# Kernel tuning notes

Hardware: AMD Instinct MI355X
Metric: run time of the kernel (lower is better)

Reference implementation:

```python
import jax, jax.numpy as jnp
import numpy as np
import itertools


def setup_inputs() -> dict:
    key = jax.random.key(0)
    k1, k2 = jax.random.split(key)
    # Learned 3D LUT: [3, D, D, D], values in [0,1] like an identity/learned color LUT
    lut = jax.random.uniform(k1, (3, 33, 33, 33), dtype=jnp.float32)
    # Input RGB image batch in [0,1): [B, 3, H, W]
    x = jax.random.uniform(k2, (4, 3, 1080, 1920), dtype=jnp.float32)
    return {"lut": lut, "x": x}


def reference(lut, x):
    # Faithful JAX version of the trilinear.forward CUDA kernel:
    # per-pixel 8-corner trilinear interpolation into a [3, D, D, D] LUT.
    dim = lut.shape[-1]
    binsize = 1.000001 / (dim - 1)

    r, g, b = x[:, 0], x[:, 1], x[:, 2]  # each [B, H, W]

    inv = 1.0 / binsize
    rid = jnp.floor(r * inv).astype(jnp.int32)
    gid = jnp.floor(g * inv).astype(jnp.int32)
    bid = jnp.floor(b * inv).astype(jnp.int32)
    # fractional offsets within the cell
    fr = r * inv - rid
    fg = g * inv - gid
    fb = b * inv - bid
    # clamp so id+1 stays in range (kernel assumes x in [0,1))
    rid = jnp.clip(rid, 0, dim - 2)
    gid = jnp.clip(gid, 0, dim - 2)
    bid = jnp.clip(bid, 0, dim - 2)

    # LUT layout matches flattened index id_r + id_g*dim + id_b*dim^2
    # i.e. lut[c, b_idx, g_idx, r_idx].
    out = jnp.zeros((3,) + r.shape, dtype=x.dtype)  # [3, B, H, W]
    for db, dg, dr in itertools.product((0, 1), repeat=3):
        wr = fr if dr else (1.0 - fr)
        wg = fg if dg else (1.0 - fg)
        wb = fb if db else (1.0 - fb)
        w = wr * wg * wb  # [B, H, W]
        corner = lut[:, bid + db, gid + dg, rid + dr]  # [3, B, H, W] gather
        out = out + w[None] * corner

    return jnp.transpose(out, (1, 0, 2, 3))  # [B, 3, H, W]
```

## Files before the change

kernel.cpp:

```cpp
#include <hip/hip_runtime.h>
#include <hip/hip_fp16.h>

#define P_PLANE (1080*1920)
#define LUT_C   35937
#define N_IMG   4
#define SMEM_WORDS 35937
#define SMEM_BYTES (SMEM_WORDS * 4)

typedef float fvec4 __attribute__((ext_vector_type(4)));

__device__ __forceinline__ float ub0(unsigned int e) { return (float)(e & 255u); }
__device__ __forceinline__ float ub1(unsigned int e) { return (float)((e >> 8) & 255u); }
__device__ __forceinline__ float ub2(unsigned int e) { return (float)((e >> 16) & 255u); }

__global__ __launch_bounds__(256) void build_lin_u8(const float* __restrict__ lut,
                                                    unsigned int* __restrict__ T) {
    int i = blockIdx.x * blockDim.x + threadIdx.x;
    if (i >= LUT_C) return;
    unsigned int r = (unsigned int)__float2int_rn(lut[i] * 255.0f);
    unsigned int g = (unsigned int)__float2int_rn(lut[LUT_C + i] * 255.0f);
    unsigned int b = (unsigned int)__float2int_rn(lut[2 * LUT_C + i] * 255.0f);
    T[i] = r | (g << 8) | (b << 16);
}

__global__ __launch_bounds__(1024, 4) void apply_lut_lds(const float* __restrict__ x,
                                                         const unsigned int* __restrict__ T,
                                                         float* __restrict__ out) {
    extern __shared__ unsigned int s_lut[];
    const int tid = threadIdx.x;

    {
        const uint4* Tv = (const uint4*)T;
        uint4* sv = (uint4*)s_lut;
        for (int i = tid; i < SMEM_WORDS / 4; i += blockDim.x) sv[i] = Tv[i];
        if (tid == 0) s_lut[SMEM_WORDS - 1] = T[SMEM_WORDS - 1];
    }
    __syncthreads();

    const float inv = (float)(1.0 / (1.000001 / 32.0));
    const float qs = 1.0f / 255.0f;
    const int QPI = P_PLANE / 4;
    const int total = N_IMG * QPI;
    const int G = gridDim.x * blockDim.x;

    int q = blockIdx.x * blockDim.x + tid;
    if (q >= total) return;

    size_t base;
    {
        int n = q / QPI;
        base = (size_t)n * (3 * P_PLANE) + (size_t)(q - n * QPI) * 4;
    }
    fvec4 r4 = *(const fvec4*)(x + base);
    fvec4 g4 = *(const fvec4*)(x + base + P_PLANE);
    fvec4 b4 = *(const fvec4*)(x + base + 2 * P_PLANE);

    while (true) {
        int   idx[4];
        float fr[4], fg[4], fb[4];
#pragma unroll
        for (int i = 0; i < 4; ++i) {
            float tr = r4[i] * inv, tg = g4[i] * inv, tb = b4[i] * inv;
            float fr_ = floorf(tr), fg_ = floorf(tg), fb_ = floorf(tb);
            fr[i] = tr - fr_; fg[i] = tg - fg_; fb[i] = tb - fb_;
            int ri = min(max((int)fr_, 0), 31);
            int gi = min(max((int)fg_, 0), 31);
            int bi = min(max((int)fb_, 0), 31);
            idx[i] = bi * 1089 + gi * 33 + ri;
        }

        unsigned int e[4][8];
#pragma unroll
        for (int i = 0; i < 4; ++i) {
            int i0 = idx[i];
            int i1 = idx[i] + 1089;
            e[i][0] = s_lut[i0];       e[i][1] = s_lut[i0 + 1];
            e[i][2] = s_lut[i0 + 33];  e[i][3] = s_lut[i0 + 34];
            e[i][4] = s_lut[i1];       e[i][5] = s_lut[i1 + 1];
            e[i][6] = s_lut[i1 + 33];  e[i][7] = s_lut[i1 + 34];
        }

        int qn = q + G;
        const bool more = (qn < total);
        int qc = more ? qn : q;
        size_t nbase;
        {
            int n = qc / QPI;
            nbase = (size_t)n * (3 * P_PLANE) + (size_t)(qc - n * QPI) * 4;
        }
        fvec4 nr4 = *(const fvec4*)(x + nbase);
        fvec4 ng4 = *(const fvec4*)(x + nbase + P_PLANE);
        fvec4 nb4 = *(const fvec4*)(x + nbase + 2 * P_PLANE);

        __builtin_amdgcn_sched_barrier(0);

        float w[4][8];
#pragma unroll
        for (int i = 0; i < 4; ++i) {
            float wr1 = fr[i], wr0 = 1.0f - fr[i];
            float wg1 = fg[i], wg0 = 1.0f - fg[i];
            float wb1 = fb[i] * qs, wb0 = (1.0f - fb[i]) * qs;
            float w00 = wb0 * wg0, w01 = wb0 * wg1, w10 = wb1 * wg0, w11 = wb1 * wg1;
            w[i][0] = w00 * wr0; w[i][1] = w00 * wr1;
            w[i][2] = w01 * wr0; w[i][3] = w01 * wr1;
            w[i][4] = w10 * wr0; w[i][5] = w10 * wr1;
            w[i][6] = w11 * wr0; w[i][7] = w11 * wr1;
        }

        fvec4 vR, vG, vB;
#pragma unroll
        for (int i = 0; i < 4; ++i) {
            float aR = w[i][0] * ub0(e[i][0]);
            float aG = w[i][0] * ub1(e[i][0]);
            float aB = w[i][0] * ub2(e[i][0]);
#pragma unroll
            for (int k = 1; k < 8; ++k) {
                aR = fmaf(w[i][k], ub0(e[i][k]), aR);
                aG = fmaf(w[i][k], ub1(e[i][k]), aG);
                aB = fmaf(w[i][k], ub2(e[i][k]), aB);
            }
            vR[i] = aR; vG[i] = aG; vB[i] = aB;
        }

        __builtin_nontemporal_store(vR, (fvec4*)(out + base));
        __builtin_nontemporal_store(vG, (fvec4*)(out + base + P_PLANE));
        __builtin_nontemporal_store(vB, (fvec4*)(out + base + 2 * P_PLANE));

        if (!more) break;
        q = qn; base = nbase;
        r4 = nr4; g4 = ng4; b4 = nb4;
    }
}

__global__ __launch_bounds__(256) void build_table(const float* __restrict__ lut,
                                                   uint4* __restrict__ T) {
    int cell = blockIdx.x * blockDim.x + threadIdx.x;
    int rid = cell & 31;
    int gid = (cell >> 5) & 31;
    int bid = cell >> 10;
    const float* b0 = lut + bid * 1089 + gid * 33 + rid;
    uint4 q[4];
    __half* h = (__half*)q;
#pragma unroll
    for (int k = 0; k < 8; ++k) {
        int off = (k >> 2) * 1089 + ((k >> 1) & 1) * 33 + (k & 1);
        h[k * 4 + 0] = __float2half(b0[off]);
        h[k * 4 + 1] = __float2half(b0[LUT_C + off]);
        h[k * 4 + 2] = __float2half(b0[2 * LUT_C + off]);
        h[k * 4 + 3] = __float2half(0.0f);
    }
    uint4* dst = T + (size_t)cell * 4;
    dst[0] = q[0]; dst[1] = q[1]; dst[2] = q[2]; dst[3] = q[3];
}

__device__ __forceinline__ void acc_chunk(const uint4& q, float wA, float wB,
                                          float& aR, float& aG, float& aB) {
    const __half* h = (const __half*)&q;
    aR = fmaf(wA, __half2float(h[0]), fmaf(wB, __half2float(h[4]), aR));
    aG = fmaf(wA, __half2float(h[1]), fmaf(wB, __half2float(h[5]), aG));
    aB = fmaf(wA, __half2float(h[2]), fmaf(wB, __half2float(h[6]), aB));
}

__global__ __launch_bounds__(256) void apply_lut(const float* __restrict__ x,
                                                 const __half* __restrict__ T,
                                                 float* __restrict__ out) {
    const float inv = (float)(1.0 / (1.000001 / 32.0));
    int n  = blockIdx.y;
    int i4 = blockIdx.x * blockDim.x + threadIdx.x;
    size_t base = (size_t)n * 3 * P_PLANE + (size_t)i4 * 4;

    float4 r4 = *(const float4*)(x + base);
    float4 g4 = *(const float4*)(x + base + P_PLANE);
    float4 b4 = *(const float4*)(x + base + 2 * P_PLANE);

    float r[4] = {r4.x, r4.y, r4.z, r4.w};
    float g[4] = {g4.x, g4.y, g4.z, g4.w};
    float b[4] = {b4.x, b4.y, b4.z, b4.w};
    float oR[4], oG[4], oB[4];

#pragma unroll
    for (int i = 0; i < 4; ++i) {
        float tr = r[i] * inv;
        float tg = g[i] * inv;
        float tb = b[i] * inv;
        float fr_ = floorf(tr), fg_ = floorf(tg), fb_ = floorf(tb);
        float fr = tr - fr_, fg = tg - fg_, fb = tb - fb_;
        int ri = min(max((int)fr_, 0), 31);
        int gi = min(max((int)fg_, 0), 31);
        int bi = min(max((int)fb_, 0), 31);

        const uint4* cp = (const uint4*)(T + ((size_t)(((bi << 5) | gi) << 5 | ri) << 5));
        uint4 q0 = cp[0], q1 = cp[1], q2 = cp[2], q3 = cp[3];

        float wr1 = fr, wr0 = 1.0f - fr;
        float wg1 = fg, wg0 = 1.0f - fg;
        float wb1 = fb, wb0 = 1.0f - fb;
        float w00 = wb0 * wg0, w01 = wb0 * wg1, w10 = wb1 * wg0, w11 = wb1 * wg1;

        float aR = 0.f, aG = 0.f, aB = 0.f;
        acc_chunk(q0, w00 * wr0, w00 * wr1, aR, aG, aB);
        acc_chunk(q1, w01 * wr0, w01 * wr1, aR, aG, aB);
        acc_chunk(q2, w10 * wr0, w10 * wr1, aR, aG, aB);
        acc_chunk(q3, w11 * wr0, w11 * wr1, aR, aG, aB);

        oR[i] = aR; oG[i] = aG; oB[i] = aB;
    }

    *(float4*)(out + base)               = make_float4(oR[0], oR[1], oR[2], oR[3]);
    *(float4*)(out + base + P_PLANE)     = make_float4(oG[0], oG[1], oG[2], oG[3]);
    *(float4*)(out + base + 2 * P_PLANE) = make_float4(oB[0], oB[1], oB[2], oB[3]);
}

extern "C" void kernel_launch(void* const* d_in, const int* in_sizes, int n_in,
                              void* d_out, int out_size, void* d_ws, size_t ws_size,
                              hipStream_t stream) {
    const float* lut = (const float*)d_in[0];
    const float* x   = (const float*)d_in[1];
    float* out = (float*)d_out;

    static int max_shm = -1;
    if (max_shm < 0) {
        int dev = 0;
        (void)hipGetDevice(&dev);
        (void)hipDeviceGetAttribute(&max_shm, hipDeviceAttributeMaxSharedMemoryPerBlock, dev);
        static_assert(SMEM_BYTES == 143748, "lut lds size");
        (void)hipFuncSetAttribute((const void*)apply_lut_lds,
                                  hipFuncAttributeMaxDynamicSharedMemorySize, SMEM_BYTES);
        if (max_shm < 0) max_shm = 0;
    }

    if (max_shm >= SMEM_BYTES && ws_size >= (size_t)SMEM_BYTES) {
        unsigned int* T = (unsigned int*)d_ws;
        build_lin_u8<<<(LUT_C + 255) / 256, 256, 0, stream>>>(lut, T);
        apply_lut_lds<<<256, 1024, SMEM_BYTES, stream>>>(x, T, out);
    } else {
        __half* T = (__half*)d_ws;
        build_table<<<128, 256, 0, stream>>>(lut, (uint4*)T);
        apply_lut<<<dim3(P_PLANE / (4 * 256), N_IMG), 256, 0, stream>>>(x, T, out);
    }
}
```

Measured before the change: 186.1 us.

## Replace static grid-stride loop with atomic-counter dynamic wavefront work stealing

Each wavefront now claims 64-quad groups from one of eight global atomic counters, one per block partition, instead of walking a fixed grid-stride sequence. The goal is to balance work across blocks and CUs, since the static split leaves some blocks finishing late (tail imbalance). The counters are zeroed inside the LUT build kernel and placed in the workspace after the table. The cost is one atomic per wavefront per iteration plus readfirstlane, and counter contention, and the workspace must now be larger.

```diff
diff --git a/kernel.cpp b/kernel.cpp
--- a/kernel.cpp
+++ b/kernel.cpp
@@ -7,6 +7,16 @@
 #define SMEM_WORDS 35937
 #define SMEM_BYTES (SMEM_WORDS * 4)
 
+#define QPI        (P_PLANE / 4)
+#define TOTAL_Q    (N_IMG * QPI)
+#define N_GROUPS   (TOTAL_Q / 64)
+#define GRP_PER_IMG (QPI / 64)
+#define N_CTR      8
+#define SPAN       (N_GROUPS / N_CTR)
+#define CTR_WORD0  36000
+#define CTR_STRIDE 64
+#define WS_NEEDED  (CTR_WORD0*4 + N_CTR*CTR_STRIDE*4)
+
 typedef float fvec4 __attribute__((ext_vector_type(4)));
 
 __device__ __forceinline__ float ub0(unsigned int e) { return (float)(e & 255u); }
@@ -14,17 +24,20 @@
 __device__ __forceinline__ float ub2(unsigned int e) { return (float)((e >> 16) & 255u); }
 
 __global__ __launch_bounds__(256) void build_lin_u8(const float* __restrict__ lut,
-                                                    unsigned int* __restrict__ T) {
+                                                    unsigned int* __restrict__ ws) {
     int i = blockIdx.x * blockDim.x + threadIdx.x;
+    if (blockIdx.x == 0 && threadIdx.x < N_CTR)
+        ws[CTR_WORD0 + threadIdx.x * CTR_STRIDE] = 0u;
     if (i >= LUT_C) return;
     unsigned int r = (unsigned int)__float2int_rn(lut[i] * 255.0f);
     unsigned int g = (unsigned int)__float2int_rn(lut[LUT_C + i] * 255.0f);
     unsigned int b = (unsigned int)__float2int_rn(lut[2 * LUT_C + i] * 255.0f);
-    T[i] = r | (g << 8) | (b << 16);
+    ws[i] = r | (g << 8) | (b << 16);
 }
 
 __global__ __launch_bounds__(1024, 4) void apply_lut_lds(const float* __restrict__ x,
                                                          const unsigned int* __restrict__ T,
+                                                         unsigned int* __restrict__ ctrs,
                                                          float* __restrict__ out) {
     extern __shared__ unsigned int s_lut[];
     const int tid = threadIdx.x;
@@ -39,23 +52,33 @@
 
     const float inv = (float)(1.0 / (1.000001 / 32.0));
     const float qs = 1.0f / 255.0f;
-    const int QPI = P_PLANE / 4;
-    const int total = N_IMG * QPI;
-    const int G = gridDim.x * blockDim.x;
-
-    int q = blockIdx.x * blockDim.x + tid;
-    if (q >= total) return;
+    const int lane = tid & 63;
+    const int c = blockIdx.x & (N_CTR - 1);
+    unsigned int* myctr = ctrs + c * CTR_STRIDE;
+    const int gbase = c * SPAN;
+
+    int t;
+    {
+        unsigned int tv = 0u;
+        if (lane == 0) tv = atomicAdd(myctr, 1u);
+        t = __builtin_amdgcn_readfirstlane((int)tv);
+    }
+    if (t >= SPAN) return;
 
     size_t base;
     {
-        int n = q / QPI;
-        base = (size_t)n * (3 * P_PLANE) + (size_t)(q - n * QPI) * 4;
+        int g = gbase + t;
+        int n = g / GRP_PER_IMG;
+        base = (size_t)n * (3 * P_PLANE) + (size_t)(g - n * GRP_PER_IMG) * 256 + lane * 4;
     }
     fvec4 r4 = *(const fvec4*)(x + base);
     fvec4 g4 = *(const fvec4*)(x + base + P_PLANE);
     fvec4 b4 = *(const fvec4*)(x + base + 2 * P_PLANE);
 
     while (true) {
+        unsigned int tv = 0u;
+        if (lane == 0) tv = atomicAdd(myctr, 1u);
+
         int   idx[4];
         float fr[4], fg[4], fb[4];
 #pragma unroll
@@ -80,13 +103,13 @@
             e[i][6] = s_lut[i1 + 33];  e[i][7] = s_lut[i1 + 34];
         }
 
-        int qn = q + G;
-        const bool more = (qn < total);
-        int qc = more ? qn : q;
+        int tn = __builtin_amdgcn_readfirstlane((int)tv);
+        const bool more = (tn < SPAN);
         size_t nbase;
         {
-            int n = qc / QPI;
-            nbase = (size_t)n * (3 * P_PLANE) + (size_t)(qc - n * QPI) * 4;
+            int g = gbase + (more ? tn : t);
+            int n = g / GRP_PER_IMG;
+            nbase = (size_t)n * (3 * P_PLANE) + (size_t)(g - n * GRP_PER_IMG) * 256 + lane * 4;
         }
         fvec4 nr4 = *(const fvec4*)(x + nbase);
         fvec4 ng4 = *(const fvec4*)(x + nbase + P_PLANE);
@@ -127,7 +150,7 @@
         __builtin_nontemporal_store(vB, (fvec4*)(out + base + 2 * P_PLANE));
 
         if (!more) break;
-        q = qn; base = nbase;
+        t = tn; base = nbase;
         r4 = nr4; g4 = ng4; b4 = nb4;
     }
 }
@@ -224,15 +247,16 @@
         (void)hipGetDevice(&dev);
         (void)hipDeviceGetAttribute(&max_shm, hipDeviceAttributeMaxSharedMemoryPerBlock, dev);
         static_assert(SMEM_BYTES == 143748, "lut lds size");
+        static_assert(N_GROUPS == 32400 && SPAN * N_CTR == N_GROUPS, "group math");
         (void)hipFuncSetAttribute((const void*)apply_lut_lds,
                                   hipFuncAttributeMaxDynamicSharedMemorySize, SMEM_BYTES);
         if (max_shm < 0) max_shm = 0;
     }
 
-    if (max_shm >= SMEM_BYTES && ws_size >= (size_t)SMEM_BYTES) {
-        unsigned int* T = (unsigned int*)d_ws;
-        build_lin_u8<<<(LUT_C + 255) / 256, 256, 0, stream>>>(lut, T);
-        apply_lut_lds<<<256, 1024, SMEM_BYTES, stream>>>(x, T, out);
+    if (max_shm >= SMEM_BYTES && ws_size >= (size_t)WS_NEEDED) {
+        unsigned int* ws = (unsigned int*)d_ws;
+        build_lin_u8<<<(LUT_C + 255) / 256, 256, 0, stream>>>(lut, ws);
+        apply_lut_lds<<<256, 1024, SMEM_BYTES, stream>>>(x, ws, ws + CTR_WORD0, out);
     } else {
         __half* T = (__half*)d_ws;
         build_table<<<128, 256, 0, stream>>>(lut, (uint4*)T);
```

New measurement: 219.2 us. 17.7% more time.
